# Optimization experiments

Hardware: AMD Instinct MI355X
Metric: run time of the kernel (lower is better)

Reference implementation:

```python
import jax, jax.numpy as jnp
import numpy as np

E = 800_000      # number of edges
DIN = 128        # in_channels
DMID = 256       # mid_channels
DOUT = 128       # output_channels
V = 50_000       # number of vertices (segments)


def setup_inputs() -> dict:
    key = jax.random.key(0)
    k1, k2, k3, k4, k5 = jax.random.split(key, 5)
    x = jax.random.normal(k1, (E, DIN), dtype=jnp.float32)
    vertex_id = jax.random.randint(k2, (E,), 0, V)
    W1 = jax.random.normal(k3, (DIN, DMID), dtype=jnp.float32) * (1.0 / np.sqrt(DIN))
    b1 = jax.random.normal(k4, (DMID,), dtype=jnp.float32) * 0.01
    W2 = jax.random.normal(k5, (DIN + DMID, DOUT), dtype=jnp.float32) * (1.0 / np.sqrt(DIN + DMID))
    return {"x": x, "vertex_id": vertex_id, "W1": W1, "b1": b1, "W2": W2, "num_vertices": V}


def reference(x, vertex_id, W1, b1, W2, num_vertices):
    # first_process: Linear(DIN -> DMID)                        (E, DMID)
    z = x @ W1 + b1
    # aggregator: scatter_max over vertex segments              (V, DMID)
    z_max = jax.ops.segment_max(z, vertex_id, num_segments=num_vertices)
    # formatter: index_select gather back to edges              (E, DMID)
    z_vertex = jnp.take(z_max, vertex_id, axis=0)
    # merger: concat along feature dim                          (E, DIN+DMID)
    z_merged = jnp.concatenate([x, z_vertex], axis=-1)
    # second_process: Linear(DIN+DMID -> DOUT, bias=False)      (E, DOUT)
    return z_merged @ W2
```

## Files before the change

kernel.cpp:

```cpp
#include <hip/hip_runtime.h>

#define DIN   128
#define DMID  256
#define DOUT  128
#define VNUM  50000

typedef __attribute__((ext_vector_type(8))) __bf16 bf16x8;
typedef __attribute__((ext_vector_type(4))) float  f32x4;

static __device__ __forceinline__ unsigned short b16(float f) {
  union { __bf16 b; unsigned short u; } r; r.b = (__bf16)f; return r.u;
}
static __device__ __forceinline__ unsigned pk2(float lo, float hi) {
  union { __bf16 b[2]; unsigned u; } r;
  r.b[0] = (__bf16)lo; r.b[1] = (__bf16)hi;
  return r.u;
}
static __device__ __forceinline__ unsigned unflip_bits(unsigned m) {
  unsigned mask = ((int)m < 0) ? 0x80000000u : 0xFFFFFFFFu;
  return m ^ mask;
}
static __device__ __forceinline__ unsigned flip32_from16(unsigned m) {
  return (m << 16) | ((m & 0x8000u) ? 0u : 0xFFFFu);
}

__global__ void k_hist(const int* __restrict__ vid, int* __restrict__ counts, int E) {
  int i = blockIdx.x * blockDim.x + threadIdx.x;
  if (i < E) atomicAdd(counts + vid[i], 1);
}

__global__ __launch_bounds__(256) void k_scan_red(
    const int* __restrict__ cnt, int* __restrict__ bsum, int V) {
  __shared__ int ws[4];
  const int i = blockIdx.x * 256 + threadIdx.x;
  int c = (i < V) ? cnt[i] : 0;
#pragma unroll
  for (int d = 1; d < 64; d <<= 1) c += __shfl_xor(c, d);
  if ((threadIdx.x & 63) == 0) ws[threadIdx.x >> 6] = c;
  __syncthreads();
  if (threadIdx.x == 0) bsum[blockIdx.x] = ws[0] + ws[1] + ws[2] + ws[3];
}

__global__ __launch_bounds__(256) void k_scan_top(int* __restrict__ bsum, int nb) {
  __shared__ int ws[4];
  const int tid = threadIdx.x, lane = tid & 63, wv = tid >> 6;
  int c = (tid < nb) ? bsum[tid] : 0;
  int s = c;
#pragma unroll
  for (int d = 1; d < 64; d <<= 1) {
    int u = __shfl_up(s, d, 64);
    if (lane >= d) s += u;
  }
  if (lane == 63) ws[wv] = s;
  __syncthreads();
  int off = 0;
  for (int k = 0; k < wv; ++k) off += ws[k];
  if (tid < nb) bsum[tid] = off + (s - c);
}

__global__ __launch_bounds__(256) void k_scan_fix(
    int* __restrict__ cursor, const int* __restrict__ bsum, int V) {
  __shared__ int ws[4];
  const int i = blockIdx.x * 256 + threadIdx.x;
  const int lane = threadIdx.x & 63, wv = threadIdx.x >> 6;
  int c = (i < V) ? cursor[i] : 0;
  int s = c;
#pragma unroll
  for (int d = 1; d < 64; d <<= 1) {
    int u = __shfl_up(s, d, 64);
    if (lane >= d) s += u;
  }
  if (lane == 63) ws[wv] = s;
  __syncthreads();
  int off = bsum[blockIdx.x];
  for (int k = 0; k < wv; ++k) off += ws[k];
  if (i < V) cursor[i] = off + (s - c);
}

__global__ void k_scatter(const int* __restrict__ vid, int* __restrict__ cursor,
                          int* __restrict__ sorted, int E) {
  int i = blockIdx.x * blockDim.x + threadIdx.x;
  if (i < E) {
    int v = vid[i];
    int p = atomicAdd(cursor + v, 1);
    sorted[p] = i;
  }
}

__global__ __launch_bounds__(512) void k_gemm1_max(
    const float* __restrict__ x, const int* __restrict__ vid,
    const int* __restrict__ sorted, const float* __restrict__ W1,
    const float* __restrict__ b1, unsigned* __restrict__ zu, int ntiles) {
  __shared__ unsigned short lx[64 * 136];
  __shared__ unsigned short zt[256 * 70];
  __shared__ int lvid[2][64];

  const int tid  = threadIdx.x;
  const int lane = tid & 63;
  const int w    = tid >> 6;
  const int l15  = lane & 15;
  const int l4   = lane >> 4;
  const int row8 = tid >> 3;
  const int s8   = tid & 7;
  const int G    = gridDim.x;

  bf16x8 bfrag[4][2];
  float  bias[2];
#pragma unroll
  for (int ni = 0; ni < 2; ++ni) {
    const int col = w * 32 + ni * 16 + l15;
    bias[ni] = b1[col];
#pragma unroll
    for (int kk = 0; kk < 4; ++kk) {
      union { bf16x8 v; unsigned short u[8]; } tmp;
#pragma unroll
      for (int j = 0; j < 8; ++j)
        tmp.u[j] = b16(W1[(kk * 32 + l4 * 8 + j) * DMID + col]);
      bfrag[kk][ni] = tmp.v;
    }
  }

  const int t0 = blockIdx.x;
  if (t0 >= ntiles) return;

  {
    if (tid < 64) lvid[0][tid] = vid[sorted[t0 * 64 + tid]];
    const int eid = sorted[t0 * 64 + row8];
    const float4* src =
        reinterpret_cast<const float4*>(x + (size_t)eid * DIN + s8 * 16);
#pragma unroll
    for (int i = 0; i < 4; ++i) {
      float4 v = src[i];
      uint2 o = { pk2(v.x, v.y), pk2(v.z, v.w) };
      *reinterpret_cast<uint2*>(&lx[row8 * 136 + s8 * 16 + i * 4]) = o;
    }
  }
  __syncthreads();

  int cur = 0;
  for (int t = t0; t < ntiles; t += G, cur ^= 1) {
    const int tn = t + G;
    const bool more = (tn < ntiles);
    int eidN = 0, sidN = 0;
    if (more) {
      eidN = sorted[tn * 64 + row8];
      if (tid < 64) sidN = sorted[tn * 64 + tid];
    }

    const int myv = lvid[cur][lane];
    const int nv  = (lane == 63) ? (myv ^ 1) : lvid[cur][lane + 1];
    const unsigned long long emask = __ballot(myv != nv);
    const bool contOpen = (lvid[cur][31] == lvid[cur][32]);

    f32x4 acc[4][2];
#pragma unroll
    for (int mi = 0; mi < 4; ++mi)
#pragma unroll
      for (int ni = 0; ni < 2; ++ni)
        acc[mi][ni] = (f32x4){bias[ni], bias[ni], bias[ni], bias[ni]};
#pragma unroll
    for (int kk = 0; kk < 4; ++kk) {
      bf16x8 a[4];
#pragma unroll
      for (int mi = 0; mi < 4; ++mi)
        a[mi] = *reinterpret_cast<const bf16x8*>(
            &lx[(mi * 16 + l15) * 136 + kk * 32 + l4 * 8]);
#pragma unroll
      for (int mi = 0; mi < 4; ++mi)
#pragma unroll
        for (int ni = 0; ni < 2; ++ni)
          acc[mi][ni] = __builtin_amdgcn_mfma_f32_16x16x32_bf16(
              a[mi], bfrag[kk][ni], acc[mi][ni], 0, 0, 0);
    }

    {
      unsigned* ztw = reinterpret_cast<unsigned*>(zt);
#pragma unroll
      for (int ni = 0; ni < 2; ++ni) {
        const int col = w * 32 + ni * 16 + l15;
        const int cb  = col * 35 + l4 * 2;
#pragma unroll
        for (int mi = 0; mi < 4; ++mi)
#pragma unroll
          for (int p = 0; p < 2; ++p) {
            unsigned tpk = pk2(acc[mi][ni][2 * p], acc[mi][ni][2 * p + 1]);
            unsigned mflip = 0x80008000u + ((tpk >> 15) & 0x00010001u) * 0x7FFFu;
            ztw[cb + mi * 8 + p] = tpk ^ mflip;
          }
      }
    }
    __syncthreads();

    float4 x0, x1, x2, x3;
    int vN = 0;
    if (more) {
      const float4* src =
          reinterpret_cast<const float4*>(x + (size_t)eidN * DIN + s8 * 16);
      x0 = src[0]; x1 = src[1]; x2 = src[2]; x3 = src[3];
      if (tid < 64) vN = vid[sidN];
    }

    {
      const int col = tid & 255;
      const int h   = tid >> 8;
      const unsigned* zc = reinterpret_cast<const unsigned*>(&zt[col * 70 + h * 32]);
      unsigned curm = 0;
      bool first = true;
#pragma unroll
      for (int p = 0; p < 16; ++p) {
        const unsigned pr = zc[p];
#pragma unroll
        for (int j = 0; j < 2; ++j) {
          const unsigned val = j ? (pr >> 16) : (pr & 0xFFFFu);
          curm = val > curm ? val : curm;
          const int row = h * 32 + p * 2 + j;
          if ((emask >> row) & 1) {
            const int v = lvid[cur][row];
            const unsigned enc = flip32_from16(curm);
            unsigned* ad = zu + (size_t)v * DMID + col;
            if (row == 63 || (first && (h == 0 || contOpen))) atomicMax(ad, enc);
            else *ad = enc;
            curm = 0; first = false;
          }
        }
      }
      if (h == 0 && !((emask >> 31) & 1)) {
        const int v = lvid[cur][31];
        atomicMax(zu + (size_t)v * DMID + col, flip32_from16(curm));
      }
    }

    if (more) {
      uint2 o0 = { pk2(x0.x, x0.y), pk2(x0.z, x0.w) };
      uint2 o1 = { pk2(x1.x, x1.y), pk2(x1.z, x1.w) };
      uint2 o2 = { pk2(x2.x, x2.y), pk2(x2.z, x2.w) };
      uint2 o3 = { pk2(x3.x, x3.y), pk2(x3.z, x3.w) };
      unsigned short* dst = &lx[row8 * 136 + s8 * 16];
      *reinterpret_cast<uint2*>(dst + 0)  = o0;
      *reinterpret_cast<uint2*>(dst + 4)  = o1;
      *reinterpret_cast<uint2*>(dst + 8)  = o2;
      *reinterpret_cast<uint2*>(dst + 12) = o3;
      if (tid < 64) lvid[cur ^ 1][tid] = vN;
    }
    __syncthreads();
  }
}

__global__ __launch_bounds__(256) void k_ymm(
    const unsigned* __restrict__ zu, const float* __restrict__ W2,
    float* __restrict__ Y, int ntiles) {
  extern __shared__ unsigned short sm[];
  unsigned short* w2bt = sm;
  unsigned short* za   = sm + 128 * 264;

  const int tid  = threadIdx.x;
  const int lane = tid & 63;
  const int w    = tid >> 6;
  const int wr   = w >> 1, wc = w & 1;
  const int l15  = lane & 15, l4 = lane >> 4;

  {
    const int n = tid & 127, kh = tid >> 7;
    for (int k = kh * 128; k < kh * 128 + 128; ++k)
      w2bt[n * 264 + k] = b16(W2[(size_t)(DIN + k) * DOUT + n]);
  }
  __syncthreads();

  for (int t = blockIdx.x; t < ntiles; t += gridDim.x) {
    {
      const int row = tid >> 2, q = tid & 3;
      const int v = t * 64 + row;
      unsigned short* dz = &za[row * 264 + q * 64];
      if (v < VNUM) {
        const uint4* sz = reinterpret_cast<const uint4*>(zu + (size_t)v * DMID + q * 64);
#pragma unroll
        for (int i = 0; i < 16; ++i) {
          uint4 m = sz[i];
          ushort4 o = { (unsigned short)(unflip_bits(m.x) >> 16),
                        (unsigned short)(unflip_bits(m.y) >> 16),
                        (unsigned short)(unflip_bits(m.z) >> 16),
                        (unsigned short)(unflip_bits(m.w) >> 16) };
          *reinterpret_cast<ushort4*>(dz + i * 4) = o;
        }
      } else {
        ushort4 zo = {0, 0, 0, 0};
#pragma unroll
        for (int i = 0; i < 16; ++i) *reinterpret_cast<ushort4*>(dz + i * 4) = zo;
      }
    }
    __syncthreads();

    f32x4 acc[2][4];
#pragma unroll
    for (int mi = 0; mi < 2; ++mi)
#pragma unroll
      for (int ni = 0; ni < 4; ++ni) acc[mi][ni] = (f32x4){0.f, 0.f, 0.f, 0.f};

#pragma unroll
    for (int kk = 0; kk < 8; ++kk) {
      bf16x8 a[2], b[4];
#pragma unroll
      for (int mi = 0; mi < 2; ++mi)
        a[mi] = *reinterpret_cast<const bf16x8*>(
            &za[(wr * 32 + mi * 16 + l15) * 264 + kk * 32 + l4 * 8]);
#pragma unroll
      for (int ni = 0; ni < 4; ++ni)
        b[ni] = *reinterpret_cast<const bf16x8*>(
            &w2bt[(wc * 64 + ni * 16 + l15) * 264 + kk * 32 + l4 * 8]);
#pragma unroll
      for (int mi = 0; mi < 2; ++mi)
#pragma unroll
        for (int ni = 0; ni < 4; ++ni)
          acc[mi][ni] = __builtin_amdgcn_mfma_f32_16x16x32_bf16(
              a[mi], b[ni], acc[mi][ni], 0, 0, 0);
    }

#pragma unroll
    for (int mi = 0; mi < 2; ++mi)
#pragma unroll
      for (int r = 0; r < 4; ++r) {
        const int v = t * 64 + wr * 32 + mi * 16 + l4 * 4 + r;
        if (v < VNUM) {
          float* o = Y + (size_t)v * DOUT + wc * 64 + l15;
#pragma unroll
          for (int ni = 0; ni < 4; ++ni) o[ni * 16] = acc[mi][ni][r];
        }
      }
    __syncthreads();
  }
}

__global__ __launch_bounds__(256, 3) void k_gemm2(
    const float* __restrict__ x, const int* __restrict__ vid,
    const float* __restrict__ W2, const float* __restrict__ Y,
    float* __restrict__ out, int ntiles) {
  __shared__ unsigned short w2at[128 * 136];
  __shared__ unsigned short lx[64 * 136];
  __shared__ int lvid[64];

  const int tid  = threadIdx.x;
  const int lane = tid & 63;
  const int w    = tid >> 6;
  const int wr   = w >> 1, wc = w & 1;
  const int l15  = lane & 15, l4 = lane >> 4;

  {
    const int n = tid & 127, kh = tid >> 7;
    for (int k = kh * 64; k < kh * 64 + 64; ++k)
      w2at[n * 136 + k] = b16(W2[(size_t)k * DOUT + n]);
  }
  __syncthreads();

  for (int t = blockIdx.x; t < ntiles; t += gridDim.x) {
    {
      const int row = tid >> 2, q = tid & 3;
      const float4* sx =
          reinterpret_cast<const float4*>(x + (size_t)(t * 64 + row) * DIN + q * 32);
#pragma unroll
      for (int i = 0; i < 8; ++i) {
        float4 v = sx[i];
        uint2 o = { pk2(v.x, v.y), pk2(v.z, v.w) };
        *reinterpret_cast<uint2*>(&lx[row * 136 + q * 32 + i * 4]) = o;
      }
      if (tid < 64) lvid[tid] = vid[t * 64 + tid];
    }
    __syncthreads();

    f32x4 acc[2][4];
#pragma unroll
    for (int mi = 0; mi < 2; ++mi)
#pragma unroll
      for (int ni = 0; ni < 4; ++ni) acc[mi][ni] = (f32x4){0.f, 0.f, 0.f, 0.f};

#pragma unroll
    for (int kk = 0; kk < 4; ++kk) {
      bf16x8 a[2], b[4];
#pragma unroll
      for (int mi = 0; mi < 2; ++mi)
        a[mi] = *reinterpret_cast<const bf16x8*>(
            &lx[(wr * 32 + mi * 16 + l15) * 136 + kk * 32 + l4 * 8]);
#pragma unroll
      for (int ni = 0; ni < 4; ++ni)
        b[ni] = *reinterpret_cast<const bf16x8*>(
            &w2at[(wc * 64 + ni * 16 + l15) * 136 + kk * 32 + l4 * 8]);
#pragma unroll
      for (int mi = 0; mi < 2; ++mi)
#pragma unroll
        for (int ni = 0; ni < 4; ++ni)
          acc[mi][ni] = __builtin_amdgcn_mfma_f32_16x16x32_bf16(
              a[mi], b[ni], acc[mi][ni], 0, 0, 0);
    }

#pragma unroll
    for (int mi = 0; mi < 2; ++mi)
#pragma unroll
      for (int r = 0; r < 4; ++r) {
        const int row = wr * 32 + mi * 16 + l4 * 4 + r;
        const float* Yr = Y + (size_t)lvid[row] * DOUT + wc * 64 + l15;
        float* o = out + (size_t)(t * 64 + row) * DOUT + wc * 64 + l15;
#pragma unroll
        for (int ni = 0; ni < 4; ++ni) o[ni * 16] = acc[mi][ni][r] + Yr[ni * 16];
      }
    __syncthreads();
  }
}

extern "C" void kernel_launch(void* const* d_in, const int* in_sizes, int n_in,
                              void* d_out, int out_size, void* d_ws, size_t ws_size,
                              hipStream_t stream) {
  const float* x   = (const float*)d_in[0];
  const int*   vid = (const int*)d_in[1];
  const float* W1  = (const float*)d_in[2];
  const float* b1  = (const float*)d_in[3];
  const float* W2  = (const float*)d_in[4];
  float* out = (float*)d_out;

  const int E = in_sizes[1];
  const int ntiles = E / 64;
  const int ntY = (VNUM + 63) / 64;
  const int nb = (VNUM + 255) / 256;

  char* ws = (char*)d_ws;
  size_t off = 0;
  unsigned* zu = (unsigned*)(ws + off); off += (size_t)VNUM * DMID * 4;
  int* cnt     = (int*)(ws + off);      off += (size_t)VNUM * 4;
  int* sorted  = (int*)(ws + off);      off += (size_t)E * 4;
  float* Y     = (float*)(ws + off);    off += (size_t)VNUM * DOUT * 4;
  int* bsum    = (int*)(ws + off);      off += 256 * 4;

  hipMemsetAsync(zu, 0, (size_t)VNUM * DMID * 4 + VNUM * 4, stream);

  k_hist<<<(E + 255) / 256, 256, 0, stream>>>(vid, cnt, E);
  k_scan_red<<<nb, 256, 0, stream>>>(cnt, bsum, VNUM);
  k_scan_top<<<1, 256, 0, stream>>>(bsum, nb);
  k_scan_fix<<<nb, 256, 0, stream>>>(cnt, bsum, VNUM);
  k_scatter<<<(E + 255) / 256, 256, 0, stream>>>(vid, cnt, sorted, E);

  k_gemm1_max<<<2048, 512, 0, stream>>>(x, vid, sorted, W1, b1, zu, ntiles);

  const int smY = (128 * 264 + 64 * 264) * sizeof(unsigned short);
  hipFuncSetAttribute((const void*)k_ymm,
                      hipFuncAttributeMaxDynamicSharedMemorySize, smY);
  k_ymm<<<782, 256, smY, stream>>>(zu, W2, Y, ntY);

  k_gemm2<<<768, 256, 0, stream>>>(x, vid, W2, Y, out, ntiles);
}
```

Measured before the change: 608.4 us.

## Pre-convert x to bf16 once and deepen gather prefetch in gemm1

Adds a conversion kernel that writes x as bf16 into the workspace when space allows, so that both gemm1's gathered loads and gemm2's streaming loads read half the bytes and skip the per-tile conversion. gemm1's software pipeline is also deepened: the sorted indices are fetched two tiles ahead, and the next tile's x loads are issued before the MFMA work instead of after it. The trade is an extra full pass that reads x in fp32 and writes it in bf16, plus more live registers in gemm1. If the workspace is too small, the code falls back to the old fp32 path.

```diff
diff --git a/kernel.cpp b/kernel.cpp
--- a/kernel.cpp
+++ b/kernel.cpp
@@ -22,6 +22,18 @@
 }
 static __device__ __forceinline__ unsigned flip32_from16(unsigned m) {
   return (m << 16) | ((m & 0x8000u) ? 0u : 0xFFFFu);
+}
+
+__global__ __launch_bounds__(256) void k_conv(
+    const float* __restrict__ x, unsigned short* __restrict__ xb, long n8) {
+  const long stride = (long)gridDim.x * blockDim.x;
+  const float4* xf = reinterpret_cast<const float4*>(x);
+  uint4* xo = reinterpret_cast<uint4*>(xb);
+  for (long k = (long)blockIdx.x * blockDim.x + threadIdx.x; k < n8; k += stride) {
+    float4 a = xf[2 * k], b = xf[2 * k + 1];
+    uint4 o = { pk2(a.x, a.y), pk2(a.z, a.w), pk2(b.x, b.y), pk2(b.z, b.w) };
+    xo[k] = o;
+  }
 }
 
 __global__ void k_hist(const int* __restrict__ vid, int* __restrict__ counts, int E) {
@@ -88,9 +100,10 @@
 }
 
 __global__ __launch_bounds__(512) void k_gemm1_max(
-    const float* __restrict__ x, const int* __restrict__ vid,
-    const int* __restrict__ sorted, const float* __restrict__ W1,
-    const float* __restrict__ b1, unsigned* __restrict__ zu, int ntiles) {
+    const float* __restrict__ x, const unsigned short* __restrict__ xbf,
+    const int* __restrict__ vid, const int* __restrict__ sorted,
+    const float* __restrict__ W1, const float* __restrict__ b1,
+    unsigned* __restrict__ zu, int ntiles) {
   __shared__ unsigned short lx[64 * 136];
   __shared__ unsigned short zt[256 * 70];
   __shared__ int lvid[2][64];
@@ -126,25 +139,47 @@
   {
     if (tid < 64) lvid[0][tid] = vid[sorted[t0 * 64 + tid]];
     const int eid = sorted[t0 * 64 + row8];
-    const float4* src =
-        reinterpret_cast<const float4*>(x + (size_t)eid * DIN + s8 * 16);
-#pragma unroll
-    for (int i = 0; i < 4; ++i) {
-      float4 v = src[i];
-      uint2 o = { pk2(v.x, v.y), pk2(v.z, v.w) };
-      *reinterpret_cast<uint2*>(&lx[row8 * 136 + s8 * 16 + i * 4]) = o;
-    }
+    uint4 A0, A1;
+    if (xbf) {
+      const uint4* s = reinterpret_cast<const uint4*>(xbf + (size_t)eid * DIN + s8 * 16);
+      A0 = s[0]; A1 = s[1];
+    } else {
+      const float4* s = reinterpret_cast<const float4*>(x + (size_t)eid * DIN + s8 * 16);
+      float4 a = s[0], b = s[1], c = s[2], d = s[3];
+      A0 = (uint4){ pk2(a.x, a.y), pk2(a.z, a.w), pk2(b.x, b.y), pk2(b.z, b.w) };
+      A1 = (uint4){ pk2(c.x, c.y), pk2(c.z, c.w), pk2(d.x, d.y), pk2(d.z, d.w) };
+    }
+    uint4* dst = reinterpret_cast<uint4*>(&lx[row8 * 136 + s8 * 16]);
+    dst[0] = A0; dst[1] = A1;
+  }
+  bool more = (t0 + G) < ntiles;
+  int eidN = 0, sidN = 0;
+  if (more) {
+    eidN = sorted[(t0 + G) * 64 + row8];
+    if (tid < 64) sidN = sorted[(t0 + G) * 64 + tid];
   }
   __syncthreads();
 
   int cur = 0;
   for (int t = t0; t < ntiles; t += G, cur ^= 1) {
-    const int tn = t + G;
-    const bool more = (tn < ntiles);
-    int eidN = 0, sidN = 0;
+    uint4 A0, A1; int vN = 0;
     if (more) {
-      eidN = sorted[tn * 64 + row8];
-      if (tid < 64) sidN = sorted[tn * 64 + tid];
+      if (xbf) {
+        const uint4* s = reinterpret_cast<const uint4*>(xbf + (size_t)eidN * DIN + s8 * 16);
+        A0 = s[0]; A1 = s[1];
+      } else {
+        const float4* s = reinterpret_cast<const float4*>(x + (size_t)eidN * DIN + s8 * 16);
+        float4 a = s[0], b = s[1], c = s[2], d = s[3];
+        A0 = (uint4){ pk2(a.x, a.y), pk2(a.z, a.w), pk2(b.x, b.y), pk2(b.z, b.w) };
+        A1 = (uint4){ pk2(c.x, c.y), pk2(c.z, c.w), pk2(d.x, d.y), pk2(d.z, d.w) };
+      }
+      if (tid < 64) vN = vid[sidN];
+    }
+    const bool more2 = (t + 2 * G) < ntiles;
+    int eidN2 = 0, sidN2 = 0;
+    if (more2) {
+      eidN2 = sorted[(t + 2 * G) * 64 + row8];
+      if (tid < 64) sidN2 = sorted[(t + 2 * G) * 64 + tid];
     }
 
     const int myv = lvid[cur][lane];
@@ -190,15 +225,6 @@
       }
     }
     __syncthreads();
-
-    float4 x0, x1, x2, x3;
-    int vN = 0;
-    if (more) {
-      const float4* src =
-          reinterpret_cast<const float4*>(x + (size_t)eidN * DIN + s8 * 16);
-      x0 = src[0]; x1 = src[1]; x2 = src[2]; x3 = src[3];
-      if (tid < 64) vN = vid[sidN];
-    }
 
     {
       const int col = tid & 255;
@@ -231,17 +257,11 @@
     }
 
     if (more) {
-      uint2 o0 = { pk2(x0.x, x0.y), pk2(x0.z, x0.w) };
-      uint2 o1 = { pk2(x1.x, x1.y), pk2(x1.z, x1.w) };
-      uint2 o2 = { pk2(x2.x, x2.y), pk2(x2.z, x2.w) };
-      uint2 o3 = { pk2(x3.x, x3.y), pk2(x3.z, x3.w) };
-      unsigned short* dst = &lx[row8 * 136 + s8 * 16];
-      *reinterpret_cast<uint2*>(dst + 0)  = o0;
-      *reinterpret_cast<uint2*>(dst + 4)  = o1;
-      *reinterpret_cast<uint2*>(dst + 8)  = o2;
-      *reinterpret_cast<uint2*>(dst + 12) = o3;
+      uint4* dst = reinterpret_cast<uint4*>(&lx[row8 * 136 + s8 * 16]);
+      dst[0] = A0; dst[1] = A1;
       if (tid < 64) lvid[cur ^ 1][tid] = vN;
     }
+    eidN = eidN2; sidN = sidN2; more = more2;
     __syncthreads();
   }
 }
@@ -331,9 +351,9 @@
 }
 
 __global__ __launch_bounds__(256, 3) void k_gemm2(
-    const float* __restrict__ x, const int* __restrict__ vid,
-    const float* __restrict__ W2, const float* __restrict__ Y,
-    float* __restrict__ out, int ntiles) {
+    const float* __restrict__ x, const unsigned short* __restrict__ xbf,
+    const int* __restrict__ vid, const float* __restrict__ W2,
+    const float* __restrict__ Y, float* __restrict__ out, int ntiles) {
   __shared__ unsigned short w2at[128 * 136];
   __shared__ unsigned short lx[64 * 136];
   __shared__ int lvid[64];
@@ -354,13 +374,22 @@
   for (int t = blockIdx.x; t < ntiles; t += gridDim.x) {
     {
       const int row = tid >> 2, q = tid & 3;
-      const float4* sx =
-          reinterpret_cast<const float4*>(x + (size_t)(t * 64 + row) * DIN + q * 32);
-#pragma unroll
-      for (int i = 0; i < 8; ++i) {
-        float4 v = sx[i];
-        uint2 o = { pk2(v.x, v.y), pk2(v.z, v.w) };
-        *reinterpret_cast<uint2*>(&lx[row * 136 + q * 32 + i * 4]) = o;
+      unsigned short* dx = &lx[row * 136 + q * 32];
+      if (xbf) {
+        const uint4* sx =
+            reinterpret_cast<const uint4*>(xbf + (size_t)(t * 64 + row) * DIN + q * 32);
+#pragma unroll
+        for (int i = 0; i < 4; ++i)
+          *reinterpret_cast<uint4*>(dx + i * 8) = sx[i];
+      } else {
+        const float4* sx =
+            reinterpret_cast<const float4*>(x + (size_t)(t * 64 + row) * DIN + q * 32);
+#pragma unroll
+        for (int i = 0; i < 8; ++i) {
+          float4 v = sx[i];
+          uint2 o = { pk2(v.x, v.y), pk2(v.z, v.w) };
+          *reinterpret_cast<uint2*>(dx + i * 4) = o;
+        }
       }
       if (tid < 64) lvid[tid] = vid[t * 64 + tid];
     }
@@ -426,9 +455,15 @@
   int* cnt     = (int*)(ws + off);      off += (size_t)VNUM * 4;
   int* sorted  = (int*)(ws + off);      off += (size_t)E * 4;
   float* Y     = (float*)(ws + off);    off += (size_t)VNUM * DOUT * 4;
-  int* bsum    = (int*)(ws + off);      off += 256 * 4;
+  int* bsum    = (int*)(ws + off);      off += 4096;
+  const size_t xb_bytes = (size_t)E * DIN * 2;
+  unsigned short* xb = (ws_size >= off + xb_bytes)
+                           ? (unsigned short*)(ws + off) : nullptr;
 
   hipMemsetAsync(zu, 0, (size_t)VNUM * DMID * 4 + VNUM * 4, stream);
+
+  if (xb)
+    k_conv<<<2048, 256, 0, stream>>>(x, xb, (long)E * DIN / 8);
 
   k_hist<<<(E + 255) / 256, 256, 0, stream>>>(vid, cnt, E);
   k_scan_red<<<nb, 256, 0, stream>>>(cnt, bsum, VNUM);
@@ -436,12 +471,12 @@
   k_scan_fix<<<nb, 256, 0, stream>>>(cnt, bsum, VNUM);
   k_scatter<<<(E + 255) / 256, 256, 0, stream>>>(vid, cnt, sorted, E);
 
-  k_gemm1_max<<<2048, 512, 0, stream>>>(x, vid, sorted, W1, b1, zu, ntiles);
+  k_gemm1_max<<<2048, 512, 0, stream>>>(x, xb, vid, sorted, W1, b1, zu, ntiles);
 
   const int smY = (128 * 264 + 64 * 264) * sizeof(unsigned short);
   hipFuncSetAttribute((const void*)k_ymm,
                       hipFuncAttributeMaxDynamicSharedMemorySize, smY);
   k_ymm<<<782, 256, smY, stream>>>(zu, W2, Y, ntY);
 
-  k_gemm2<<<768, 256, 0, stream>>>(x, vid, W2, Y, out, ntiles);
-}
+  k_gemm2<<<768, 256, 0, stream>>>(x, xb, vid, W2, Y, out, ntiles);
+}
```

Measured after the change: 681.0 us. 1.12x slower.

## Split gemm1 columns across four blocks and drop software prefetch pipeline

Applied to the files above, without the earlier changes.

The first GEMM plus segment-max kernel now runs with 256-thread blocks, each owning a 64-column slice of the 256 mid channels, with four column-group blocks per row tile. Each tile's reduction splits rows into four 16-row segments instead of two 32-row halves, using a boundary check to decide between atomic and plain stores. The double-buffered prefetch of the next tile's x rows is removed in favour of a simple load, sync, compute loop. This lowers per-block LDS and registers to raise occupancy, at the cost of each x tile being gathered and converted four times and more atomic boundary writes.

```diff
diff --git a/kernel.cpp b/kernel.cpp
--- a/kernel.cpp
+++ b/kernel.cpp
@@ -87,28 +87,31 @@
   }
 }
 
-__global__ __launch_bounds__(512) void k_gemm1_max(
+__global__ __launch_bounds__(256) void k_gemm1_max(
     const float* __restrict__ x, const int* __restrict__ vid,
     const int* __restrict__ sorted, const float* __restrict__ W1,
     const float* __restrict__ b1, unsigned* __restrict__ zu, int ntiles) {
-  __shared__ unsigned short lx[64 * 136];
-  __shared__ unsigned short zt[256 * 70];
-  __shared__ int lvid[2][64];
+  __shared__ unsigned short lx[64 * 132];
+  __shared__ unsigned short zt[64 * 68];
+  __shared__ int lvid[64];
 
   const int tid  = threadIdx.x;
   const int lane = tid & 63;
   const int w    = tid >> 6;
+  const int wr   = w & 1;
+  const int wc   = w >> 1;
   const int l15  = lane & 15;
   const int l4   = lane >> 4;
-  const int row8 = tid >> 3;
-  const int s8   = tid & 7;
-  const int G    = gridDim.x;
+  const int row4 = tid >> 2;
+  const int s4   = tid & 3;
+  const int colbase = (blockIdx.x & 3) * 64;
+  const int tstep   = gridDim.x >> 2;
 
   bf16x8 bfrag[4][2];
   float  bias[2];
 #pragma unroll
   for (int ni = 0; ni < 2; ++ni) {
-    const int col = w * 32 + ni * 16 + l15;
+    const int col = colbase + wc * 32 + ni * 16 + l15;
     bias[ni] = b1[col];
 #pragma unroll
     for (int kk = 0; kk < 4; ++kk) {
@@ -120,53 +123,41 @@
     }
   }
 
-  const int t0 = blockIdx.x;
-  if (t0 >= ntiles) return;
-
-  {
-    if (tid < 64) lvid[0][tid] = vid[sorted[t0 * 64 + tid]];
-    const int eid = sorted[t0 * 64 + row8];
-    const float4* src =
-        reinterpret_cast<const float4*>(x + (size_t)eid * DIN + s8 * 16);
-#pragma unroll
-    for (int i = 0; i < 4; ++i) {
-      float4 v = src[i];
-      uint2 o = { pk2(v.x, v.y), pk2(v.z, v.w) };
-      *reinterpret_cast<uint2*>(&lx[row8 * 136 + s8 * 16 + i * 4]) = o;
-    }
-  }
-  __syncthreads();
-
-  int cur = 0;
-  for (int t = t0; t < ntiles; t += G, cur ^= 1) {
-    const int tn = t + G;
-    const bool more = (tn < ntiles);
-    int eidN = 0, sidN = 0;
-    if (more) {
-      eidN = sorted[tn * 64 + row8];
-      if (tid < 64) sidN = sorted[tn * 64 + tid];
-    }
-
-    const int myv = lvid[cur][lane];
-    const int nv  = (lane == 63) ? (myv ^ 1) : lvid[cur][lane + 1];
+  for (int t = blockIdx.x >> 2; t < ntiles; t += tstep) {
+    if (tid < 64) lvid[tid] = vid[sorted[t * 64 + tid]];
+    {
+      const int eid = sorted[t * 64 + row4];
+      const float4* src =
+          reinterpret_cast<const float4*>(x + (size_t)eid * DIN + s4 * 32);
+      unsigned short* dst = &lx[row4 * 132 + s4 * 32];
+#pragma unroll
+      for (int i = 0; i < 8; ++i) {
+        float4 v = src[i];
+        uint2 o = { pk2(v.x, v.y), pk2(v.z, v.w) };
+        *reinterpret_cast<uint2*>(dst + i * 4) = o;
+      }
+    }
+    __syncthreads();
+
+    const int myv = lvid[lane];
+    const int nv  = (lane == 63) ? (myv ^ 1) : lvid[lane + 1];
     const unsigned long long emask = __ballot(myv != nv);
-    const bool contOpen = (lvid[cur][31] == lvid[cur][32]);
-
-    f32x4 acc[4][2];
-#pragma unroll
-    for (int mi = 0; mi < 4; ++mi)
+
+    f32x4 acc[2][2];
+#pragma unroll
+    for (int mi = 0; mi < 2; ++mi)
 #pragma unroll
       for (int ni = 0; ni < 2; ++ni)
         acc[mi][ni] = (f32x4){bias[ni], bias[ni], bias[ni], bias[ni]};
 #pragma unroll
     for (int kk = 0; kk < 4; ++kk) {
-      bf16x8 a[4];
-#pragma unroll
-      for (int mi = 0; mi < 4; ++mi)
+      bf16x8 a[2];
+#pragma unroll
+      for (int mi = 0; mi < 2; ++mi)
         a[mi] = *reinterpret_cast<const bf16x8*>(
-            &lx[(mi * 16 + l15) * 136 + kk * 32 + l4 * 8]);
-#pragma unroll
-      for (int mi = 0; mi < 4; ++mi)
+            &lx[(wr * 32 + mi * 16 + l15) * 132 + kk * 32 + l4 * 8]);
+#pragma unroll
+      for (int mi = 0; mi < 2; ++mi)
 #pragma unroll
         for (int ni = 0; ni < 2; ++ni)
           acc[mi][ni] = __builtin_amdgcn_mfma_f32_16x16x32_bf16(
@@ -177,10 +168,10 @@
       unsigned* ztw = reinterpret_cast<unsigned*>(zt);
 #pragma unroll
       for (int ni = 0; ni < 2; ++ni) {
-        const int col = w * 32 + ni * 16 + l15;
-        const int cb  = col * 35 + l4 * 2;
-#pragma unroll
-        for (int mi = 0; mi < 4; ++mi)
+        const int colb = wc * 32 + ni * 16 + l15;
+        const int cb = colb * 34 + wr * 16 + l4 * 2;
+#pragma unroll
+        for (int mi = 0; mi < 2; ++mi)
 #pragma unroll
           for (int p = 0; p < 2; ++p) {
             unsigned tpk = pk2(acc[mi][ni][2 * p], acc[mi][ni][2 * p + 1]);
@@ -191,56 +182,35 @@
     }
     __syncthreads();
 
-    float4 x0, x1, x2, x3;
-    int vN = 0;
-    if (more) {
-      const float4* src =
-          reinterpret_cast<const float4*>(x + (size_t)eidN * DIN + s8 * 16);
-      x0 = src[0]; x1 = src[1]; x2 = src[2]; x3 = src[3];
-      if (tid < 64) vN = vid[sidN];
-    }
-
     {
-      const int col = tid & 255;
-      const int h   = tid >> 8;
-      const unsigned* zc = reinterpret_cast<const unsigned*>(&zt[col * 70 + h * 32]);
-      unsigned curm = 0;
+      const int c64 = tid & 63;
+      const int q   = tid >> 6;
+      const int col = colbase + c64;
+      const unsigned* zc =
+          reinterpret_cast<const unsigned*>(&zt[c64 * 68 + q * 16]);
+      unsigned cur = 0;
       bool first = true;
-#pragma unroll
-      for (int p = 0; p < 16; ++p) {
+      const bool extL = (q == 0) ? true : (lvid[q * 16 - 1] == lvid[q * 16]);
+#pragma unroll
+      for (int p = 0; p < 8; ++p) {
         const unsigned pr = zc[p];
 #pragma unroll
         for (int j = 0; j < 2; ++j) {
           const unsigned val = j ? (pr >> 16) : (pr & 0xFFFFu);
-          curm = val > curm ? val : curm;
-          const int row = h * 32 + p * 2 + j;
+          cur = val > cur ? val : cur;
+          const int row = q * 16 + p * 2 + j;
           if ((emask >> row) & 1) {
-            const int v = lvid[cur][row];
-            const unsigned enc = flip32_from16(curm);
-            unsigned* ad = zu + (size_t)v * DMID + col;
-            if (row == 63 || (first && (h == 0 || contOpen))) atomicMax(ad, enc);
+            const unsigned enc = flip32_from16(cur);
+            unsigned* ad = zu + (size_t)lvid[row] * DMID + col;
+            if ((first && extL) || row == 63) atomicMax(ad, enc);
             else *ad = enc;
-            curm = 0; first = false;
+            cur = 0; first = false;
           }
         }
       }
-      if (h == 0 && !((emask >> 31) & 1)) {
-        const int v = lvid[cur][31];
-        atomicMax(zu + (size_t)v * DMID + col, flip32_from16(curm));
-      }
-    }
-
-    if (more) {
-      uint2 o0 = { pk2(x0.x, x0.y), pk2(x0.z, x0.w) };
-      uint2 o1 = { pk2(x1.x, x1.y), pk2(x1.z, x1.w) };
-      uint2 o2 = { pk2(x2.x, x2.y), pk2(x2.z, x2.w) };
-      uint2 o3 = { pk2(x3.x, x3.y), pk2(x3.z, x3.w) };
-      unsigned short* dst = &lx[row8 * 136 + s8 * 16];
-      *reinterpret_cast<uint2*>(dst + 0)  = o0;
-      *reinterpret_cast<uint2*>(dst + 4)  = o1;
-      *reinterpret_cast<uint2*>(dst + 8)  = o2;
-      *reinterpret_cast<uint2*>(dst + 12) = o3;
-      if (tid < 64) lvid[cur ^ 1][tid] = vN;
+      if (!((emask >> (q * 16 + 15)) & 1))
+        atomicMax(zu + (size_t)lvid[q * 16 + 15] * DMID + col,
+                  flip32_from16(cur));
     }
     __syncthreads();
   }
@@ -426,7 +396,7 @@
   int* cnt     = (int*)(ws + off);      off += (size_t)VNUM * 4;
   int* sorted  = (int*)(ws + off);      off += (size_t)E * 4;
   float* Y     = (float*)(ws + off);    off += (size_t)VNUM * DOUT * 4;
-  int* bsum    = (int*)(ws + off);      off += 256 * 4;
+  int* bsum    = (int*)(ws + off);      off += 4096;
 
   hipMemsetAsync(zu, 0, (size_t)VNUM * DMID * 4 + VNUM * 4, stream);
 
@@ -436,7 +406,7 @@
   k_scan_fix<<<nb, 256, 0, stream>>>(cnt, bsum, VNUM);
   k_scatter<<<(E + 255) / 256, 256, 0, stream>>>(vid, cnt, sorted, E);
 
-  k_gemm1_max<<<2048, 512, 0, stream>>>(x, vid, sorted, W1, b1, zu, ntiles);
+  k_gemm1_max<<<4096, 256, 0, stream>>>(x, vid, sorted, W1, b1, zu, ntiles);
 
   const int smY = (128 * 264 + 64 * 264) * sizeof(unsigned short);
   hipFuncSetAttribute((const void*)k_ymm,
```

Result: slower. 743.9 us (+22.3%).

## Materialize vertex-sorted bf16 copy of x during scatter, stream it in GEMM1

Applied to the files above, without the earlier changes.

The scatter kernel now writes a bf16 copy of each edge's x row and its vertex id directly into sorted position, using one atomic per edge broadcast across 8 lanes. GEMM1 then reads contiguous bf16 rows and sorted vertex ids instead of gathering fp32 rows through an index array. This replaces the dependent random gathers in the GEMM loop with coalesced streaming reads. In exchange it adds an extra write and read of an E×128 bf16 buffer plus a scattered write pass.

```diff
diff --git a/kernel.cpp b/kernel.cpp
--- a/kernel.cpp
+++ b/kernel.cpp
@@ -77,20 +77,33 @@
   if (i < V) cursor[i] = off + (s - c);
 }
 
-__global__ void k_scatter(const int* __restrict__ vid, int* __restrict__ cursor,
-                          int* __restrict__ sorted, int E) {
-  int i = blockIdx.x * blockDim.x + threadIdx.x;
-  if (i < E) {
-    int v = vid[i];
-    int p = atomicAdd(cursor + v, 1);
-    sorted[p] = i;
-  }
+__global__ __launch_bounds__(256) void k_scatter_copy(
+    const float* __restrict__ x, const int* __restrict__ vid,
+    int* __restrict__ cursor, unsigned short* __restrict__ xs,
+    int* __restrict__ svid, int E) {
+  const int g = blockIdx.x * 256 + threadIdx.x;
+  const int e = g >> 3;
+  if (e >= E) return;
+  const int lane = threadIdx.x & 63;
+  const int s8 = g & 7;
+  const int v = vid[e];
+  int p = 0;
+  if (s8 == 0) p = atomicAdd(cursor + v, 1);
+  p = __shfl(p, (lane >> 3) << 3, 64);
+
+  const float4* src = reinterpret_cast<const float4*>(x + (size_t)e * DIN + s8 * 16);
+  float4 a = src[0], b = src[1], c = src[2], d = src[3];
+  uint4 o0 = { pk2(a.x, a.y), pk2(a.z, a.w), pk2(b.x, b.y), pk2(b.z, b.w) };
+  uint4 o1 = { pk2(c.x, c.y), pk2(c.z, c.w), pk2(d.x, d.y), pk2(d.z, d.w) };
+  uint4* dst = reinterpret_cast<uint4*>(xs + (size_t)p * DIN + s8 * 16);
+  dst[0] = o0; dst[1] = o1;
+  if (s8 == 0) svid[p] = v;
 }
 
 __global__ __launch_bounds__(512) void k_gemm1_max(
-    const float* __restrict__ x, const int* __restrict__ vid,
-    const int* __restrict__ sorted, const float* __restrict__ W1,
-    const float* __restrict__ b1, unsigned* __restrict__ zu, int ntiles) {
+    const unsigned short* __restrict__ xs, const int* __restrict__ svid,
+    const float* __restrict__ W1, const float* __restrict__ b1,
+    unsigned* __restrict__ zu, int ntiles) {
   __shared__ unsigned short lx[64 * 136];
   __shared__ unsigned short zt[256 * 70];
   __shared__ int lvid[2][64];
@@ -124,27 +137,24 @@
   if (t0 >= ntiles) return;
 
   {
-    if (tid < 64) lvid[0][tid] = vid[sorted[t0 * 64 + tid]];
-    const int eid = sorted[t0 * 64 + row8];
-    const float4* src =
-        reinterpret_cast<const float4*>(x + (size_t)eid * DIN + s8 * 16);
-#pragma unroll
-    for (int i = 0; i < 4; ++i) {
-      float4 v = src[i];
-      uint2 o = { pk2(v.x, v.y), pk2(v.z, v.w) };
-      *reinterpret_cast<uint2*>(&lx[row8 * 136 + s8 * 16 + i * 4]) = o;
-    }
+    if (tid < 64) lvid[0][tid] = svid[t0 * 64 + tid];
+    const uint4* s =
+        reinterpret_cast<const uint4*>(xs + ((size_t)t0 * 64 + row8) * DIN + s8 * 16);
+    uint4* dst = reinterpret_cast<uint4*>(&lx[row8 * 136 + s8 * 16]);
+    dst[0] = s[0]; dst[1] = s[1];
   }
   __syncthreads();
 
   int cur = 0;
   for (int t = t0; t < ntiles; t += G, cur ^= 1) {
-    const int tn = t + G;
-    const bool more = (tn < ntiles);
-    int eidN = 0, sidN = 0;
+    const bool more = (t + G) < ntiles;
+
+    uint4 A0, A1; int vN = 0;
     if (more) {
-      eidN = sorted[tn * 64 + row8];
-      if (tid < 64) sidN = sorted[tn * 64 + tid];
+      const uint4* s = reinterpret_cast<const uint4*>(
+          xs + ((size_t)(t + G) * 64 + row8) * DIN + s8 * 16);
+      A0 = s[0]; A1 = s[1];
+      if (tid < 64) vN = svid[(t + G) * 64 + tid];
     }
 
     const int myv = lvid[cur][lane];
@@ -190,15 +200,6 @@
       }
     }
     __syncthreads();
-
-    float4 x0, x1, x2, x3;
-    int vN = 0;
-    if (more) {
-      const float4* src =
-          reinterpret_cast<const float4*>(x + (size_t)eidN * DIN + s8 * 16);
-      x0 = src[0]; x1 = src[1]; x2 = src[2]; x3 = src[3];
-      if (tid < 64) vN = vid[sidN];
-    }
 
     {
       const int col = tid & 255;
@@ -231,15 +232,8 @@
     }
 
     if (more) {
-      uint2 o0 = { pk2(x0.x, x0.y), pk2(x0.z, x0.w) };
-      uint2 o1 = { pk2(x1.x, x1.y), pk2(x1.z, x1.w) };
-      uint2 o2 = { pk2(x2.x, x2.y), pk2(x2.z, x2.w) };
-      uint2 o3 = { pk2(x3.x, x3.y), pk2(x3.z, x3.w) };
-      unsigned short* dst = &lx[row8 * 136 + s8 * 16];
-      *reinterpret_cast<uint2*>(dst + 0)  = o0;
-      *reinterpret_cast<uint2*>(dst + 4)  = o1;
-      *reinterpret_cast<uint2*>(dst + 8)  = o2;
-      *reinterpret_cast<uint2*>(dst + 12) = o3;
+      uint4* dst = reinterpret_cast<uint4*>(&lx[row8 * 136 + s8 * 16]);
+      dst[0] = A0; dst[1] = A1;
       if (tid < 64) lvid[cur ^ 1][tid] = vN;
     }
     __syncthreads();
@@ -424,9 +418,10 @@
   size_t off = 0;
   unsigned* zu = (unsigned*)(ws + off); off += (size_t)VNUM * DMID * 4;
   int* cnt     = (int*)(ws + off);      off += (size_t)VNUM * 4;
-  int* sorted  = (int*)(ws + off);      off += (size_t)E * 4;
   float* Y     = (float*)(ws + off);    off += (size_t)VNUM * DOUT * 4;
-  int* bsum    = (int*)(ws + off);      off += 256 * 4;
+  int* bsum    = (int*)(ws + off);      off += 4096;
+  int* svid    = (int*)(ws + off);      off += (size_t)E * 4;
+  unsigned short* xs = (unsigned short*)(ws + off);
 
   hipMemsetAsync(zu, 0, (size_t)VNUM * DMID * 4 + VNUM * 4, stream);
 
@@ -434,9 +429,9 @@
   k_scan_red<<<nb, 256, 0, stream>>>(cnt, bsum, VNUM);
   k_scan_top<<<1, 256, 0, stream>>>(bsum, nb);
   k_scan_fix<<<nb, 256, 0, stream>>>(cnt, bsum, VNUM);
-  k_scatter<<<(E + 255) / 256, 256, 0, stream>>>(vid, cnt, sorted, E);
-
-  k_gemm1_max<<<2048, 512, 0, stream>>>(x, vid, sorted, W1, b1, zu, ntiles);
+  k_scatter_copy<<<(E * 8 + 255) / 256, 256, 0, stream>>>(x, vid, cnt, xs, svid, E);
+
+  k_gemm1_max<<<2048, 512, 0, stream>>>(xs, svid, W1, b1, zu, ntiles);
 
   const int smY = (128 * 264 + 64 * 264) * sizeof(unsigned short);
   hipFuncSetAttribute((const void*)k_ymm,
```

After: 652.7 us. 1.07x slower.
